# Optimization experiments

Hardware: AMD Instinct MI355X
Metric: run time of the kernel (lower is better)

## Reference

```python
import jax, jax.numpy as jnp
import numpy as np

T = 32400   # bs*H*W BEV queries (1*180*180)
S = 16896   # bs*num_cams*h*w image keys (1*6*32*88)
E = 256     # embed_dim
H = 8       # num_heads
D = 32      # head_dim
MAXL = 32   # max interval length (ref_num_f)


def _mlp(x, w1, b1, w2, b2):
    # nn.Sequential(Linear(E,2E), ReLU, Linear(2E,E))
    return jax.nn.relu(x @ w1 + b1) @ w2 + b2


def setup_inputs() -> dict:
    k0 = jax.random.key(0)
    ks = jax.random.split(k0, 8)
    # ragged interval structure: every BEV cell has an interval of length (idx%32)+1
    lengths = (np.arange(T) % MAXL) + 1
    starts = np.concatenate([np.zeros(1, np.int64), np.cumsum(lengths)[:-1]])
    N = int(lengths.sum())  # 534472 frustum points
    ranks_bev = np.repeat(np.arange(T), lengths)          # sorted by BEV cell
    rng = np.random.default_rng(0)
    ranks_feat = rng.integers(0, S, size=N)               # which key/value row each point reads

    def lin(k, fi, fo):
        return jax.random.normal(k, (fi, fo), jnp.float32) * (1.0 / np.sqrt(fi))

    key_feat = jax.random.normal(ks[1], (S, E), jnp.float32)
    return dict(
        query_depth=jax.random.normal(ks[0], (T, E), jnp.float32),
        key=key_feat,
        value=key_feat,  # module asserts torch.equal(key, value)
        q_w1=lin(ks[2], E, 2 * E), q_b1=jnp.zeros((2 * E,), jnp.float32),
        q_w2=lin(ks[3], 2 * E, E), q_b2=jnp.zeros((E,), jnp.float32),
        k_w1=lin(ks[4], E, 2 * E), k_b1=jnp.zeros((2 * E,), jnp.float32),
        k_w2=lin(ks[5], 2 * E, E), k_b2=jnp.zeros((E,), jnp.float32),
        ranks_feat_f=jnp.asarray(ranks_feat, jnp.int32),
        ranks_bev_f=jnp.asarray(ranks_bev, jnp.int32),
        interval_starts_f=jnp.asarray(starts, jnp.int32),
        interval_lengths_f=jnp.asarray(lengths, jnp.int32),
        ref_num=MAXL,
    )


def reference(query_depth, key, value,
              q_w1, q_b1, q_w2, q_b2,
              k_w1, k_b1, k_w2, k_b2,
              ranks_feat_f, ranks_bev_f,
              interval_starts_f, interval_lengths_f, ref_num):
    scaling = 1.0 / jnp.sqrt(jnp.float32(D))
    q = (_mlp(query_depth, q_w1, q_b1, q_w2, q_b2) * scaling).reshape(T, H, D)
    k = _mlp(key, k_w1, k_b1, k_w2, k_b2).reshape(S, H, D)
    v = value.reshape(S, H, D)

    N = ranks_bev_f.shape[0]
    pt = jnp.arange(N, dtype=jnp.int32)
    # interval id of each point (intervals are contiguous, sorted by start)
    iid = jnp.searchsorted(interval_starts_f, pt, side='right') - 1
    ranks_ref = pt - interval_starts_f[iid]  # within-interval slot, in [0, ref_num)

    # per-point raw attention logit: q[bev] . k[feat] per head  -> [N, H]
    w = jnp.einsum('nhd,nhd->nh', q[ranks_bev_f], k[ranks_feat_f])

    # scatter into ragged weight tensor [T, H, ref_num]; padding masked to -1e9
    attn = jnp.full((T, H, ref_num), -1e9, jnp.float32)
    attn = attn.at[ranks_bev_f, :, ranks_ref].set(w)
    attn = jax.nn.softmax(attn, axis=-1)

    # gather normalized weights back per point and scatter-combine values
    wp = attn[ranks_bev_f, :, ranks_ref]          # [N, H]
    vp = v[ranks_feat_f]                          # [N, H, D]
    out = jnp.zeros((T, H, D), jnp.float32).at[ranks_bev_f].add(wp[:, :, None] * vp)
    return out.reshape(T, E)
```

## Files before the change

kernel.cpp:

```cpp
#include <hip/hip_runtime.h>
#include <hip/hip_bf16.h>
#include <cstdint>
#include <cstddef>

constexpr int T_Q   = 32400;
constexpr int T_PAD = 32512;
constexpr int S_K   = 16896;
constexpr int E_DIM = 256;
constexpr int HID   = 512;

typedef __bf16 bf16x8 __attribute__((ext_vector_type(8)));
typedef float  f32x4  __attribute__((ext_vector_type(4)));

__device__ __forceinline__ void async16(const __hip_bfloat16* gp, __hip_bfloat16* lp) {
    __builtin_amdgcn_global_load_lds(
        (const __attribute__((address_space(1))) void*)(gp),
        (__attribute__((address_space(3))) void*)(lp), 16, 0, 0);
}

__device__ __forceinline__ float b2f(unsigned short u) {
    return __uint_as_float(((unsigned)u) << 16);
}

__global__ __launch_bounds__(256) void cast_pad(const float* __restrict__ src,
                                                __hip_bfloat16* __restrict__ dst,
                                                int valid, int total) {
    int i = (blockIdx.x * 256 + threadIdx.x) * 4;
    if (i >= total) return;
    float4 f = make_float4(0.f, 0.f, 0.f, 0.f);
    if (i < valid) f = *(const float4*)(src + i);
    union { ushort4 u4; __hip_bfloat16 b[4]; } cv;
    cv.b[0] = __float2bfloat16(f.x);
    cv.b[1] = __float2bfloat16(f.y);
    cv.b[2] = __float2bfloat16(f.z);
    cv.b[3] = __float2bfloat16(f.w);
    *(ushort4*)(dst + i) = cv.u4;
}

__global__ __launch_bounds__(256) void transpose_w(
    const float* __restrict__ s0, const float* __restrict__ s1,
    const float* __restrict__ s2, const float* __restrict__ s3,
    __hip_bfloat16* __restrict__ d0, __hip_bfloat16* __restrict__ d1,
    __hip_bfloat16* __restrict__ d2, __hip_bfloat16* __restrict__ d3) {
    int idx = blockIdx.x * 256 + threadIdx.x;
    int seg = idx >> 17;
    int r   = idx & ((1 << 17) - 1);
    const float* s = seg == 0 ? s0 : seg == 1 ? s1 : seg == 2 ? s2 : s3;
    __hip_bfloat16* d = seg == 0 ? d0 : seg == 1 ? d1 : seg == 2 ? d2 : d3;
    int kb = (seg & 1) ? 9 : 8;
    int n = r >> kb;
    int k = r & ((1 << kb) - 1);
    d[r] = __float2bfloat16(s[(k << (17 - kb)) + n]);
}

constexpr int BM = 128, BN = 128, BK = 32;

__global__ __launch_bounds__(256) void gemm_bf16(
    const __hip_bfloat16* __restrict__ A,
    const __hip_bfloat16* __restrict__ BT,
    const float* __restrict__ bias,
    __hip_bfloat16* __restrict__ C,
    int K, int N, int relu, float scale) {
    __shared__ __hip_bfloat16 As[BM * BK];
    __shared__ __hip_bfloat16 Bs[BN * BK];

    const int ntiles = N >> 7;
    const int tm = blockIdx.x / ntiles;
    const int tn = blockIdx.x - tm * ntiles;
    const size_t m0 = (size_t)tm * BM;
    const int n0 = tn * BN;

    const int tid = threadIdx.x;
    const int w = tid >> 6, l = tid & 63;
    const int lm = l & 15, lq = l >> 4;
    const int wm = (w >> 1) << 6, wn = (w & 1) << 6;

    const int srow = l >> 2;
    const int scol = (((l & 3) ^ (srow & 3)) << 3);

    f32x4 acc[4][4] = {};

    for (int k0 = 0; k0 < K; k0 += BK) {
#pragma unroll
        for (int c = 0; c < 2; ++c) {
            int r = c * 64 + w * 16 + srow;
            async16(A  + (m0 + r) * K + k0 + scol, As + (c * 64 + w * 16) * BK);
            async16(BT + (size_t)(n0 + r) * K + k0 + scol, Bs + (c * 64 + w * 16) * BK);
        }
        __syncthreads();

        const int rsw = ((lq ^ (lm & 3)) << 3);
        bf16x8 af[4], bfr[4];
#pragma unroll
        for (int mi = 0; mi < 4; ++mi) {
            int row = wm + mi * 16 + lm;
            af[mi] = *(const bf16x8*)(As + row * BK + rsw);
        }
#pragma unroll
        for (int ni = 0; ni < 4; ++ni) {
            int row = wn + ni * 16 + lm;
            bfr[ni] = *(const bf16x8*)(Bs + row * BK + rsw);
        }
#pragma unroll
        for (int mi = 0; mi < 4; ++mi)
#pragma unroll
            for (int ni = 0; ni < 4; ++ni)
                acc[mi][ni] = __builtin_amdgcn_mfma_f32_16x16x32_bf16(
                    af[mi], bfr[ni], acc[mi][ni], 0, 0, 0);
        __syncthreads();
    }

#pragma unroll
    for (int ni = 0; ni < 4; ++ni) {
        int col = n0 + wn + ni * 16 + lm;
        float bv = bias[col];
#pragma unroll
        for (int mi = 0; mi < 4; ++mi) {
            size_t rowb = m0 + wm + mi * 16 + lq * 4;
#pragma unroll
            for (int r = 0; r < 4; ++r) {
                float vv = acc[mi][ni][r] + bv;
                if (relu) vv = fmaxf(vv, 0.f);
                C[(rowb + r) * N + col] = __float2bfloat16(vv * scale);
            }
        }
    }
}

__global__ __launch_bounds__(256) void attn_kernel(
    const __hip_bfloat16* __restrict__ q,
    const __hip_bfloat16* __restrict__ k,
    const __hip_bfloat16* __restrict__ v,
    const int* __restrict__ ranks_feat,
    const int* __restrict__ starts,
    const int* __restrict__ lens,
    float* __restrict__ out) {
    int t = blockIdx.x * 4 + (threadIdx.x >> 6);
    if (t >= T_Q) return;
    int l = threadIdx.x & 63;
    int start = starts[t];
    int L = lens[t];

    int myf = (l < L) ? ranks_feat[start + l] : 0;

    ushort4 qu = *(const ushort4*)(q + (size_t)t * 256 + l * 4);
    float q0 = b2f(qu.x), q1 = b2f(qu.y), q2 = b2f(qu.z), q3 = b2f(qu.w);

    float m = -INFINITY, s = 0.f;
    float a0 = 0.f, a1 = 0.f, a2 = 0.f, a3 = 0.f;

    for (int j = 0; j < L; ++j) {
        int f = __shfl(myf, j);
        const __hip_bfloat16* kp = k + (size_t)f * 256 + l * 4;
        ushort4 ku = *(const ushort4*)kp;
        float wv = q0 * b2f(ku.x) + q1 * b2f(ku.y) + q2 * b2f(ku.z) + q3 * b2f(ku.w);
        wv += __shfl_xor(wv, 1);
        wv += __shfl_xor(wv, 2);
        wv += __shfl_xor(wv, 4);

        float mn = fmaxf(m, wv);
        float al = __expf(m - mn);
        float p  = __expf(wv - mn);
        s = s * al + p;

        const __hip_bfloat16* vp = v + (size_t)f * 256 + l * 4;
        ushort4 vu = *(const ushort4*)vp;
        a0 = a0 * al + p * b2f(vu.x);
        a1 = a1 * al + p * b2f(vu.y);
        a2 = a2 * al + p * b2f(vu.z);
        a3 = a3 * al + p * b2f(vu.w);
        m = mn;
    }
    float inv = 1.f / s;
    float4 o = make_float4(a0 * inv, a1 * inv, a2 * inv, a3 * inv);
    *(float4*)(out + (size_t)t * 256 + l * 4) = o;
}

extern "C" void kernel_launch(void* const* d_in, const int* in_sizes, int n_in,
                              void* d_out, int out_size, void* d_ws, size_t ws_size,
                              hipStream_t stream) {
    const float* q_in   = (const float*)d_in[0];
    const float* key_in = (const float*)d_in[1];
    const float* val_in = (const float*)d_in[2];
    const float* q_w1   = (const float*)d_in[3];
    const float* q_b1   = (const float*)d_in[4];
    const float* q_w2   = (const float*)d_in[5];
    const float* q_b2   = (const float*)d_in[6];
    const float* k_w1   = (const float*)d_in[7];
    const float* k_b1   = (const float*)d_in[8];
    const float* k_w2   = (const float*)d_in[9];
    const float* k_b2   = (const float*)d_in[10];
    const int* ranks_feat = (const int*)d_in[11];
    const int* starts     = (const int*)d_in[13];
    const int* lens       = (const int*)d_in[14];
    float* out = (float*)d_out;

    char* ws = (char*)d_ws;
    size_t off = 0;
    auto alloc = [&](size_t bytes) {
        char* p = ws + off;
        off += (bytes + 255) & ~(size_t)255;
        return p;
    };
    __hip_bfloat16* qA   = (__hip_bfloat16*)alloc((size_t)T_PAD * E_DIM * 2);
    __hip_bfloat16* hidQ = (__hip_bfloat16*)alloc((size_t)T_PAD * HID * 2);
    __hip_bfloat16* qMl  = (__hip_bfloat16*)alloc((size_t)T_PAD * E_DIM * 2);
    __hip_bfloat16* kA   = (__hip_bfloat16*)alloc((size_t)S_K * E_DIM * 2);
    __hip_bfloat16* hidK = (__hip_bfloat16*)alloc((size_t)S_K * HID * 2);
    __hip_bfloat16* kMl  = (__hip_bfloat16*)alloc((size_t)S_K * E_DIM * 2);
    __hip_bfloat16* vB   = (__hip_bfloat16*)alloc((size_t)S_K * E_DIM * 2);
    __hip_bfloat16* w1qT = (__hip_bfloat16*)alloc((size_t)HID * E_DIM * 2);
    __hip_bfloat16* w2qT = (__hip_bfloat16*)alloc((size_t)E_DIM * HID * 2);
    __hip_bfloat16* w1kT = (__hip_bfloat16*)alloc((size_t)HID * E_DIM * 2);
    __hip_bfloat16* w2kT = (__hip_bfloat16*)alloc((size_t)E_DIM * HID * 2);
    (void)ws_size; (void)n_in; (void)in_sizes; (void)out_size;

    cast_pad<<<(T_PAD * E_DIM / 4) / 256, 256, 0, stream>>>(q_in, qA, T_Q * E_DIM, T_PAD * E_DIM);
    cast_pad<<<(S_K * E_DIM / 4) / 256, 256, 0, stream>>>(key_in, kA, S_K * E_DIM, S_K * E_DIM);
    cast_pad<<<(S_K * E_DIM / 4) / 256, 256, 0, stream>>>(val_in, vB, S_K * E_DIM, S_K * E_DIM);
    transpose_w<<<2048, 256, 0, stream>>>(q_w1, q_w2, k_w1, k_w2, w1qT, w2qT, w1kT, w2kT);

    const float qscale = 0.17677669529663687f;
    gemm_bf16<<<(T_PAD / 128) * (HID / 128), 256, 0, stream>>>(qA, w1qT, q_b1, hidQ, E_DIM, HID, 1, 1.0f);
    gemm_bf16<<<(T_PAD / 128) * (E_DIM / 128), 256, 0, stream>>>(hidQ, w2qT, q_b2, qMl, HID, E_DIM, 0, qscale);
    gemm_bf16<<<(S_K / 128) * (HID / 128), 256, 0, stream>>>(kA, w1kT, k_b1, hidK, E_DIM, HID, 1, 1.0f);
    gemm_bf16<<<(S_K / 128) * (E_DIM / 128), 256, 0, stream>>>(hidK, w2kT, k_b2, kMl, HID, E_DIM, 0, 1.0f);
    attn_kernel<<<T_Q / 4, 256, 0, stream>>>(qMl, kMl, vB, ranks_feat, starts, lens, out);
}
```

Before: 326.6 us.

## Software-pipeline attention gathers in batches of four and merge prep kernels

The attention loop now processes four interval points per step with double-buffered register prefetch of K and V rows, batched online-softmax updates, and clamped index loads, so gather latency overlaps with compute instead of being serialized per point. The three cast kernels and the weight transpose are merged into one launch, and the transpose now goes through an LDS tile so reads and writes are both coalesced. The cost is higher register pressure and some wasted loads when the interval length is not a multiple of four.

Measured after the change: 318.6 us. 2.4% less time.

```diff
diff --git a/kernel.cpp b/kernel.cpp
--- a/kernel.cpp
+++ b/kernel.cpp
@@ -22,35 +22,62 @@
     return __uint_as_float(((unsigned)u) << 16);
 }
 
-__global__ __launch_bounds__(256) void cast_pad(const float* __restrict__ src,
-                                                __hip_bfloat16* __restrict__ dst,
-                                                int valid, int total) {
-    int i = (blockIdx.x * 256 + threadIdx.x) * 4;
-    if (i >= total) return;
-    float4 f = make_float4(0.f, 0.f, 0.f, 0.f);
-    if (i < valid) f = *(const float4*)(src + i);
-    union { ushort4 u4; __hip_bfloat16 b[4]; } cv;
-    cv.b[0] = __float2bfloat16(f.x);
-    cv.b[1] = __float2bfloat16(f.y);
-    cv.b[2] = __float2bfloat16(f.z);
-    cv.b[3] = __float2bfloat16(f.w);
-    *(ushort4*)(dst + i) = cv.u4;
-}
-
-__global__ __launch_bounds__(256) void transpose_w(
+constexpr int NB_Q = (T_PAD * E_DIM / 4) / 256;
+constexpr int NB_K = (S_K * E_DIM / 4) / 256;
+constexpr int NB_PREP = NB_Q + NB_K + NB_K + 128;
+
+__global__ __launch_bounds__(256) void prep(
+    const float* __restrict__ q_in, const float* __restrict__ key_in,
+    const float* __restrict__ val_in,
     const float* __restrict__ s0, const float* __restrict__ s1,
     const float* __restrict__ s2, const float* __restrict__ s3,
+    __hip_bfloat16* __restrict__ qA, __hip_bfloat16* __restrict__ kA,
+    __hip_bfloat16* __restrict__ vB,
     __hip_bfloat16* __restrict__ d0, __hip_bfloat16* __restrict__ d1,
     __hip_bfloat16* __restrict__ d2, __hip_bfloat16* __restrict__ d3) {
-    int idx = blockIdx.x * 256 + threadIdx.x;
-    int seg = idx >> 17;
-    int r   = idx & ((1 << 17) - 1);
-    const float* s = seg == 0 ? s0 : seg == 1 ? s1 : seg == 2 ? s2 : s3;
-    __hip_bfloat16* d = seg == 0 ? d0 : seg == 1 ? d1 : seg == 2 ? d2 : d3;
-    int kb = (seg & 1) ? 9 : 8;
-    int n = r >> kb;
-    int k = r & ((1 << kb) - 1);
-    d[r] = __float2bfloat16(s[(k << (17 - kb)) + n]);
+    __shared__ float tb[64][65];
+    const int b = blockIdx.x;
+    const int tid = threadIdx.x;
+
+    if (b < NB_Q + 2 * NB_K) {
+        const float* src;
+        __hip_bfloat16* dst;
+        int bl, valid;
+        if (b < NB_Q) { src = q_in; dst = qA; bl = b; valid = T_Q * E_DIM; }
+        else if (b < NB_Q + NB_K) { src = key_in; dst = kA; bl = b - NB_Q; valid = S_K * E_DIM; }
+        else { src = val_in; dst = vB; bl = b - NB_Q - NB_K; valid = S_K * E_DIM; }
+        int i = (bl * 256 + tid) * 4;
+        float4 f = make_float4(0.f, 0.f, 0.f, 0.f);
+        if (i < valid) f = *(const float4*)(src + i);
+        union { ushort4 u4; __hip_bfloat16 bb[4]; } cv;
+        cv.bb[0] = __float2bfloat16(f.x);
+        cv.bb[1] = __float2bfloat16(f.y);
+        cv.bb[2] = __float2bfloat16(f.z);
+        cv.bb[3] = __float2bfloat16(f.w);
+        *(ushort4*)(dst + i) = cv.u4;
+        return;
+    }
+
+    int tloc = b - (NB_Q + 2 * NB_K);
+    int m = tloc >> 5;
+    int tt = tloc & 31;
+    const float* S = m == 0 ? s0 : m == 1 ? s1 : m == 2 ? s2 : s3;
+    __hip_bfloat16* D = m == 0 ? d0 : m == 1 ? d1 : m == 2 ? d2 : d3;
+    int Kd, Nd, kt, nt;
+    if ((m & 1) == 0) { Kd = 256; Nd = 512; kt = tt & 3; nt = tt >> 2; }
+    else              { Kd = 512; Nd = 256; kt = tt & 7; nt = tt >> 3; }
+    int tx = tid & 63, ty = tid >> 6;
+#pragma unroll
+    for (int p = 0; p < 16; ++p) {
+        int row = ty * 16 + p;
+        tb[row][tx] = S[(size_t)(kt * 64 + row) * Nd + nt * 64 + tx];
+    }
+    __syncthreads();
+#pragma unroll
+    for (int p = 0; p < 16; ++p) {
+        int row = ty * 16 + p;
+        D[(size_t)(nt * 64 + row) * Kd + kt * 64 + tx] = __float2bfloat16(tb[tx][row]);
+    }
 }
 
 constexpr int BM = 128, BN = 128, BK = 32;
@@ -92,15 +119,11 @@
         const int rsw = ((lq ^ (lm & 3)) << 3);
         bf16x8 af[4], bfr[4];
 #pragma unroll
-        for (int mi = 0; mi < 4; ++mi) {
-            int row = wm + mi * 16 + lm;
-            af[mi] = *(const bf16x8*)(As + row * BK + rsw);
-        }
-#pragma unroll
-        for (int ni = 0; ni < 4; ++ni) {
-            int row = wn + ni * 16 + lm;
-            bfr[ni] = *(const bf16x8*)(Bs + row * BK + rsw);
-        }
+        for (int mi = 0; mi < 4; ++mi)
+            af[mi] = *(const bf16x8*)(As + (wm + mi * 16 + lm) * BK + rsw);
+#pragma unroll
+        for (int ni = 0; ni < 4; ++ni)
+            bfr[ni] = *(const bf16x8*)(Bs + (wn + ni * 16 + lm) * BK + rsw);
 #pragma unroll
         for (int mi = 0; mi < 4; ++mi)
 #pragma unroll
@@ -127,53 +150,90 @@
     }
 }
 
+#define PREF(K0,K1,K2,K3,V0,V1,V2,V3,J0)                                    \
+    {                                                                        \
+        int j_ = (J0);                                                       \
+        int i0 = su + j_ + 0; i0 = i0 < nmax ? i0 : nmax;                    \
+        int i1 = su + j_ + 1; i1 = i1 < nmax ? i1 : nmax;                    \
+        int i2 = su + j_ + 2; i2 = i2 < nmax ? i2 : nmax;                    \
+        int i3 = su + j_ + 3; i3 = i3 < nmax ? i3 : nmax;                    \
+        int f0 = rf[i0], f1 = rf[i1], f2 = rf[i2], f3 = rf[i3];              \
+        K0 = *(const ushort4*)(kp + (size_t)f0 * 256 + l4);                  \
+        V0 = *(const ushort4*)(vp + (size_t)f0 * 256 + l4);                  \
+        K1 = *(const ushort4*)(kp + (size_t)f1 * 256 + l4);                  \
+        V1 = *(const ushort4*)(vp + (size_t)f1 * 256 + l4);                  \
+        K2 = *(const ushort4*)(kp + (size_t)f2 * 256 + l4);                  \
+        V2 = *(const ushort4*)(vp + (size_t)f2 * 256 + l4);                  \
+        K3 = *(const ushort4*)(kp + (size_t)f3 * 256 + l4);                  \
+        V3 = *(const ushort4*)(vp + (size_t)f3 * 256 + l4);                  \
+    }
+
+#define DOT4(K_) fmaf(q0, b2f(K_.x), fmaf(q1, b2f(K_.y), fmaf(q2, b2f(K_.z), q3 * b2f(K_.w))))
+
+#define PROC(K0,K1,K2,K3,V0,V1,V2,V3,J0)                                    \
+    {                                                                        \
+        float w0 = DOT4(K0), w1 = DOT4(K1), w2 = DOT4(K2), w3 = DOT4(K3);   \
+        w0 += __shfl_xor(w0, 1); w1 += __shfl_xor(w1, 1);                   \
+        w2 += __shfl_xor(w2, 1); w3 += __shfl_xor(w3, 1);                   \
+        w0 += __shfl_xor(w0, 2); w1 += __shfl_xor(w1, 2);                   \
+        w2 += __shfl_xor(w2, 2); w3 += __shfl_xor(w3, 2);                   \
+        w0 += __shfl_xor(w0, 4); w1 += __shfl_xor(w1, 4);                   \
+        w2 += __shfl_xor(w2, 4); w3 += __shfl_xor(w3, 4);                   \
+        if ((J0) + 1 >= L) w1 = -1e30f;                                      \
+        if ((J0) + 2 >= L) w2 = -1e30f;                                      \
+        if ((J0) + 3 >= L) w3 = -1e30f;                                      \
+        float mw = fmaxf(fmaxf(w0, w1), fmaxf(w2, w3));                      \
+        float mn = fmaxf(m, mw);                                             \
+        float al = __expf(m - mn); m = mn;                                   \
+        float p0 = __expf(w0 - mn), p1 = __expf(w1 - mn);                    \
+        float p2 = __expf(w2 - mn), p3 = __expf(w3 - mn);                    \
+        s = s * al + ((p0 + p1) + (p2 + p3));                                \
+        a0 = fmaf(p3, b2f(V3.x), fmaf(p2, b2f(V2.x), fmaf(p1, b2f(V1.x), fmaf(p0, b2f(V0.x), a0 * al)))); \
+        a1 = fmaf(p3, b2f(V3.y), fmaf(p2, b2f(V2.y), fmaf(p1, b2f(V1.y), fmaf(p0, b2f(V0.y), a1 * al)))); \
+        a2 = fmaf(p3, b2f(V3.z), fmaf(p2, b2f(V2.z), fmaf(p1, b2f(V1.z), fmaf(p0, b2f(V0.z), a2 * al)))); \
+        a3 = fmaf(p3, b2f(V3.w), fmaf(p2, b2f(V2.w), fmaf(p1, b2f(V1.w), fmaf(p0, b2f(V0.w), a3 * al)))); \
+    }
+
 __global__ __launch_bounds__(256) void attn_kernel(
     const __hip_bfloat16* __restrict__ q,
-    const __hip_bfloat16* __restrict__ k,
-    const __hip_bfloat16* __restrict__ v,
-    const int* __restrict__ ranks_feat,
+    const __hip_bfloat16* __restrict__ kp,
+    const __hip_bfloat16* __restrict__ vp,
+    const int* __restrict__ rf,
     const int* __restrict__ starts,
     const int* __restrict__ lens,
+    int nmax,
     float* __restrict__ out) {
     int t = blockIdx.x * 4 + (threadIdx.x >> 6);
     if (t >= T_Q) return;
     int l = threadIdx.x & 63;
-    int start = starts[t];
-    int L = lens[t];
-
-    int myf = (l < L) ? ranks_feat[start + l] : 0;
-
-    ushort4 qu = *(const ushort4*)(q + (size_t)t * 256 + l * 4);
+    int l4 = l * 4;
+    int su = __builtin_amdgcn_readfirstlane(starts[t]);
+    int L  = __builtin_amdgcn_readfirstlane(lens[t]);
+
+    ushort4 qu = *(const ushort4*)(q + (size_t)t * 256 + l4);
     float q0 = b2f(qu.x), q1 = b2f(qu.y), q2 = b2f(qu.z), q3 = b2f(qu.w);
 
     float m = -INFINITY, s = 0.f;
     float a0 = 0.f, a1 = 0.f, a2 = 0.f, a3 = 0.f;
 
-    for (int j = 0; j < L; ++j) {
-        int f = __shfl(myf, j);
-        const __hip_bfloat16* kp = k + (size_t)f * 256 + l * 4;
-        ushort4 ku = *(const ushort4*)kp;
-        float wv = q0 * b2f(ku.x) + q1 * b2f(ku.y) + q2 * b2f(ku.z) + q3 * b2f(ku.w);
-        wv += __shfl_xor(wv, 1);
-        wv += __shfl_xor(wv, 2);
-        wv += __shfl_xor(wv, 4);
-
-        float mn = fmaxf(m, wv);
-        float al = __expf(m - mn);
-        float p  = __expf(wv - mn);
-        s = s * al + p;
-
-        const __hip_bfloat16* vp = v + (size_t)f * 256 + l * 4;
-        ushort4 vu = *(const ushort4*)vp;
-        a0 = a0 * al + p * b2f(vu.x);
-        a1 = a1 * al + p * b2f(vu.y);
-        a2 = a2 * al + p * b2f(vu.z);
-        a3 = a3 * al + p * b2f(vu.w);
-        m = mn;
-    }
+    ushort4 ak0, ak1, ak2, ak3, av0, av1, av2, av3;
+    ushort4 bk0, bk1, bk2, bk3, bv0, bv1, bv2, bv3;
+
+    int Lr = (L + 3) & ~3;
+    PREF(ak0, ak1, ak2, ak3, av0, av1, av2, av3, 0);
+    for (int j0 = 0; j0 < Lr; j0 += 8) {
+        bool hasB = (j0 + 4 < Lr);
+        if (hasB) PREF(bk0, bk1, bk2, bk3, bv0, bv1, bv2, bv3, j0 + 4);
+        PROC(ak0, ak1, ak2, ak3, av0, av1, av2, av3, j0);
+        if (hasB) {
+            if (j0 + 8 < Lr) PREF(ak0, ak1, ak2, ak3, av0, av1, av2, av3, j0 + 8);
+            PROC(bk0, bk1, bk2, bk3, bv0, bv1, bv2, bv3, j0 + 4);
+        }
+    }
+
     float inv = 1.f / s;
     float4 o = make_float4(a0 * inv, a1 * inv, a2 * inv, a3 * inv);
-    *(float4*)(out + (size_t)t * 256 + l * 4) = o;
+    *(float4*)(out + (size_t)t * 256 + l4) = o;
 }
 
 extern "C" void kernel_launch(void* const* d_in, const int* in_sizes, int n_in,
@@ -194,6 +254,7 @@
     const int* starts     = (const int*)d_in[13];
     const int* lens       = (const int*)d_in[14];
     float* out = (float*)d_out;
+    const int n_points = in_sizes[11];
 
     char* ws = (char*)d_ws;
     size_t off = 0;
@@ -213,17 +274,18 @@
     __hip_bfloat16* w2qT = (__hip_bfloat16*)alloc((size_t)E_DIM * HID * 2);
     __hip_bfloat16* w1kT = (__hip_bfloat16*)alloc((size_t)HID * E_DIM * 2);
     __hip_bfloat16* w2kT = (__hip_bfloat16*)alloc((size_t)E_DIM * HID * 2);
-    (void)ws_size; (void)n_in; (void)in_sizes; (void)out_size;
-
-    cast_pad<<<(T_PAD * E_DIM / 4) / 256, 256, 0, stream>>>(q_in, qA, T_Q * E_DIM, T_PAD * E_DIM);
-    cast_pad<<<(S_K * E_DIM / 4) / 256, 256, 0, stream>>>(key_in, kA, S_K * E_DIM, S_K * E_DIM);
-    cast_pad<<<(S_K * E_DIM / 4) / 256, 256, 0, stream>>>(val_in, vB, S_K * E_DIM, S_K * E_DIM);
-    transpose_w<<<2048, 256, 0, stream>>>(q_w1, q_w2, k_w1, k_w2, w1qT, w2qT, w1kT, w2kT);
+    (void)ws_size; (void)n_in; (void)out_size;
+
+    prep<<<NB_PREP, 256, 0, stream>>>(q_in, key_in, val_in,
+                                      q_w1, q_w2, k_w1, k_w2,
+                                      qA, kA, vB, w1qT, w2qT, w1kT, w2kT);
 
     const float qscale = 0.17677669529663687f;
     gemm_bf16<<<(T_PAD / 128) * (HID / 128), 256, 0, stream>>>(qA, w1qT, q_b1, hidQ, E_DIM, HID, 1, 1.0f);
     gemm_bf16<<<(T_PAD / 128) * (E_DIM / 128), 256, 0, stream>>>(hidQ, w2qT, q_b2, qMl, HID, E_DIM, 0, qscale);
     gemm_bf16<<<(S_K / 128) * (HID / 128), 256, 0, stream>>>(kA, w1kT, k_b1, hidK, E_DIM, HID, 1, 1.0f);
     gemm_bf16<<<(S_K / 128) * (E_DIM / 128), 256, 0, stream>>>(hidK, w2kT, k_b2, kMl, HID, E_DIM, 0, 1.0f);
-    attn_kernel<<<T_Q / 4, 256, 0, stream>>>(qMl, kMl, vB, ranks_feat, starts, lens, out);
-}
+
+    attn_kernel<<<T_Q / 4, 256, 0, stream>>>(qMl, kMl, vB, ranks_feat, starts, lens,
+                                             n_points - 1, out);
+}
```
